# Performance work log

Hardware: AMD Instinct MI355X
Metric: run time of the kernel (lower is better)

## Reference

```python
import jax, jax.numpy as jnp
import numpy as np

B, S, D, H = 2, 2048, 1024, 16
DK = D // H


def setup_inputs() -> dict:
    key = jax.random.key(0)
    ks = jax.random.split(key, 7)
    return {
        "query": jax.random.normal(ks[0], (B, S, D), jnp.float32),
        "key": jax.random.normal(ks[1], (B, S, D), jnp.float32),
        "value": jax.random.normal(ks[2], (B, S, D), jnp.float32),
        "w_q": jax.random.normal(ks[3], (D, D), jnp.float32) * (1.0 / np.sqrt(D)),
        "w_k": jax.random.normal(ks[4], (D, D), jnp.float32) * (1.0 / np.sqrt(D)),
        "w_v": jax.random.normal(ks[5], (D, D), jnp.float32) * (1.0 / np.sqrt(D)),
        "w_o": jax.random.normal(ks[6], (D, D), jnp.float32) * (1.0 / np.sqrt(D)),
    }


def reference(query, key, value, w_q, w_k, w_v, w_o):
    # Linear(bias=False) in torch computes x @ W.T where W is [out, in].
    Q = jnp.einsum('bsd,ed->bse', query, w_q)
    K = jnp.einsum('bsd,ed->bse', key, w_k)
    V = jnp.einsum('bsd,ed->bse', value, w_v)
    # split heads: [B, H, S, DK]
    Q = Q.reshape(B, S, H, DK).transpose(0, 2, 1, 3)
    K = K.reshape(B, S, H, DK).transpose(0, 2, 1, 3)
    V = V.reshape(B, S, H, DK).transpose(0, 2, 1, 3)
    scale = 1.0 / np.sqrt(DK).astype(np.float32)
    scores = jnp.einsum('bhqd,bhkd->bhqk', Q, K) * scale  # [B,H,S,S]
    attn = jax.nn.softmax(scores, axis=-1)
    context = jnp.einsum('bhqk,bhkd->bhqd', attn, V)
    context = context.transpose(0, 2, 1, 3).reshape(B, S, D)
    return jnp.einsum('bsd,ed->bse', context, w_o)
```

## Files before the change

kernel.cpp:

```cpp
#include <hip/hip_runtime.h>

typedef unsigned short u16;
typedef unsigned int u32;
typedef __bf16 bf16x8 __attribute__((ext_vector_type(8)));
typedef float f32x4 __attribute__((ext_vector_type(4)));
typedef short s16x4 __attribute__((ext_vector_type(4)));

#define AS1 __attribute__((address_space(1)))
#define AS3 __attribute__((address_space(3)))

__device__ __forceinline__ f32x4 mfma16(bf16x8 a, bf16x8 b, f32x4 c) {
    return __builtin_amdgcn_mfma_f32_16x16x32_bf16(a, b, c, 0, 0, 0);
}
__device__ __forceinline__ f32x4 mfma16k16(s16x4 a, s16x4 b, f32x4 c) {
    return __builtin_amdgcn_mfma_f32_16x16x16bf16_1k(a, b, c, 0, 0, 0);
}

__device__ __forceinline__ u16 f2bf(float f) {
    return __builtin_bit_cast(u16, (__bf16)f);
}

__device__ __forceinline__ void gld16(const u16* g, u16* l) {
    __builtin_amdgcn_global_load_lds((AS1 void*)g, (AS3 void*)l, 16, 0, 0);
}

__global__ __launch_bounds__(256) void cvt_all(const float* __restrict__ q, const float* __restrict__ k,
                                               const float* __restrict__ v, const float* __restrict__ wq,
                                               const float* __restrict__ wk, const float* __restrict__ wv,
                                               const float* __restrict__ wo, u16* __restrict__ qo,
                                               u16* __restrict__ ko, u16* __restrict__ vo,
                                               u16* __restrict__ wqo, u16* __restrict__ wko,
                                               u16* __restrict__ wvo, u16* __restrict__ woo) {
    const int y = blockIdx.y;
    const float* x; u16* o; int n;
    switch (y) {
        case 0: x = q; o = qo; n = 4 << 20; break;
        case 1: x = k; o = ko; n = 4 << 20; break;
        case 2: x = v; o = vo; n = 4 << 20; break;
        case 3: x = wq; o = wqo; n = 1 << 20; break;
        case 4: x = wk; o = wko; n = 1 << 20; break;
        case 5: x = wv; o = wvo; n = 1 << 20; break;
        default: x = wo; o = woo; n = 1 << 20; break;
    }
    int i = (blockIdx.x * 256 + threadIdx.x) * 4;
    if (i >= n) return;
    float4 vv = *(const float4*)(x + i);
    u32 lo = (u32)f2bf(vv.x) | ((u32)f2bf(vv.y) << 16);
    u32 hi = (u32)f2bf(vv.z) | ((u32)f2bf(vv.w) << 16);
    *(uint2*)(o + i) = make_uint2(lo, hi);
}

template <int BM, int BN, bool BF16OUT>
__device__ __forceinline__ void gemm_core(const u16* __restrict__ A, const u16* __restrict__ Bt,
                                          void* __restrict__ Cp, int K, int N, int m0, int n0,
                                          float oscale) {
    constexpr int WROWS = BM / 64;
    constexpr int WCOLS = 4 / WROWS;
    constexpr int BFR = BN / WCOLS / 16;
    __shared__ __align__(16) u16 As[BM * 32];
    __shared__ __align__(16) u16 Bs[BN * 32];
    const int tid = threadIdx.x;
    const int lane = tid & 63, wave = tid >> 6;
    const int l16 = lane & 15, q4 = lane >> 4;
    const int wm = (wave / WCOLS) * 64, wn = (wave % WCOLS) * (BFR * 16);

    const f32x4 fz = {0.f, 0.f, 0.f, 0.f};
    f32x4 acc[4][BFR];
#pragma unroll
    for (int i = 0; i < 4; ++i)
#pragma unroll
        for (int j = 0; j < BFR; ++j) acc[i][j] = fz;

    const int rseg = lane >> 2;
    const int ck = ((lane & 3) ^ ((lane >> 3) & 3)) * 8;
    const u16* Ag = A + (size_t)(m0 + wave * 16 + rseg) * K + ck;
    const u16* Bg = Bt + (size_t)(n0 + wave * 16 + rseg) * K + ck;

    const int swz = (q4 ^ ((l16 & 7) >> 1)) * 8;

    for (int k0 = 0; k0 < K; k0 += 32) {
        __syncthreads();
#pragma unroll
        for (int p = 0; p < BM / 64; ++p)
            gld16(Ag + (size_t)p * 64 * K + k0, As + p * 2048 + wave * 512);
#pragma unroll
        for (int p = 0; p < BN / 64; ++p)
            gld16(Bg + (size_t)p * 64 * K + k0, Bs + p * 2048 + wave * 512);
        __syncthreads();
        bf16x8 af[4], bfr[BFR];
#pragma unroll
        for (int i = 0; i < 4; ++i)
            af[i] = *(const bf16x8*)&As[(wm + i * 16 + l16) * 32 + swz];
#pragma unroll
        for (int j = 0; j < BFR; ++j)
            bfr[j] = *(const bf16x8*)&Bs[(wn + j * 16 + l16) * 32 + swz];
#pragma unroll
        for (int i = 0; i < 4; ++i)
#pragma unroll
            for (int j = 0; j < BFR; ++j) acc[i][j] = mfma16(af[i], bfr[j], acc[i][j]);
    }

#pragma unroll
    for (int i = 0; i < 4; ++i) {
        const int row = m0 + wm + i * 16 + q4 * 4;
#pragma unroll
        for (int j = 0; j < BFR; ++j) {
            const int col = n0 + wn + j * 16 + l16;
#pragma unroll
            for (int r = 0; r < 4; ++r) {
                const float vr = acc[i][j][r] * oscale;
                if constexpr (BF16OUT)
                    ((u16*)Cp)[(size_t)(row + r) * N + col] = f2bf(vr);
                else
                    ((float*)Cp)[(size_t)(row + r) * N + col] = vr;
            }
        }
    }
}

__global__ __launch_bounds__(256) void gemm_qkv(const u16* __restrict__ qb, const u16* __restrict__ kb,
                                                const u16* __restrict__ vb, const u16* __restrict__ wqb,
                                                const u16* __restrict__ wkb, const u16* __restrict__ wvb,
                                                u16* __restrict__ Qp, u16* __restrict__ Kp,
                                                u16* __restrict__ VtAll) {
    const int z = blockIdx.y, x = blockIdx.x;
    const u16 *A, *Bt;
    u16* C;
    int N, m0, n0;
    float sc = 1.0f;
    if (z == 0) {
        A = qb; Bt = wqb; C = Qp; N = 1024; m0 = (x >> 3) * 128; n0 = (x & 7) * 128;
        sc = 0.18033688011112042f;
    } else if (z == 1) {
        A = kb; Bt = wkb; C = Kp; N = 1024; m0 = (x >> 3) * 128; n0 = (x & 7) * 128;
    } else {
        A = wvb; Bt = vb; C = VtAll; N = 4096; m0 = (x >> 5) * 128; n0 = (x & 31) * 128;
    }
    gemm_core<128, 128, true>(A, Bt, C, 1024, N, m0, n0, sc);
}

__global__ __launch_bounds__(256) void gemm_out(const u16* __restrict__ ctx,
                                                const u16* __restrict__ wob,
                                                float* __restrict__ out) {
    const int x = blockIdx.x;
    gemm_core<64, 128, false>(ctx, wob, out, 1024, 1024, (x >> 3) * 64, (x & 7) * 128, 1.0f);
}

__global__ __launch_bounds__(256) void flash_attn(const u16* __restrict__ Qp,
                                                  const u16* __restrict__ Kp,
                                                  const u16* __restrict__ VtAll,
                                                  float* __restrict__ Op0,
                                                  float* __restrict__ Op1,
                                                  float* __restrict__ Lp,
                                                  int NS, int ktLen) {
    constexpr int D = 1024, SS = 2048, LD = 72;
    __shared__ __align__(16) u16 Ks[64 * LD];
    __shared__ __align__(16) u16 Vts[64 * LD];

    const int tid = threadIdx.x;
    const int lane = tid & 63, wave = tid >> 6;
    const int l16 = lane & 15, q4 = lane >> 4;
    const int h = blockIdx.y;
    const int b = blockIdx.z / NS, half = blockIdx.z - b * NS;
    const int q0 = blockIdx.x * 128 + wave * 32;
    const int kt0 = half * ktLen, ktEnd = kt0 + ktLen;

    bf16x8 qf[2][2];
#pragma unroll
    for (int qs = 0; qs < 2; ++qs) {
        const u16* Qb = Qp + (size_t)(b * SS + q0 + qs * 16 + l16) * D + h * 64;
        qf[qs][0] = *(const bf16x8*)(Qb + q4 * 8);
        qf[qs][1] = *(const bf16x8*)(Qb + 32 + q4 * 8);
    }

    const f32x4 fz = {0.f, 0.f, 0.f, 0.f};
    f32x4 ot[2][4], lacc[2];
    lacc[0] = fz; lacc[1] = fz;
#pragma unroll
    for (int qs = 0; qs < 2; ++qs)
#pragma unroll
        for (int dt = 0; dt < 4; ++dt) ot[qs][dt] = fz;

    s16x4 onesA;
    onesA[0] = onesA[1] = onesA[2] = onesA[3] = (short)0x3F80;

    const int sr = tid >> 3, scol = (tid & 7) * 8;
    const int vswap = wave & 1;
    const int swV = (l16 >> 3) & 1;
    const u16* Kg = Kp + (size_t)(b * SS + sr) * D + h * 64 + scol;
    const u16* Vg = VtAll + (size_t)(h * 64 + sr) * 4096 + b * SS + scol;

    uint4 k0v = *(const uint4*)(Kg + (size_t)kt0 * D);
    uint4 k1v = *(const uint4*)(Kg + (size_t)(kt0 + 32) * D);
    uint4 v0v = *(const uint4*)(Vg + kt0);
    uint4 v1v = *(const uint4*)(Vg + (size_t)32 * 4096 + kt0);

    for (int kt = kt0; kt < ktEnd; kt += 64) {
        if (vswap) {
            v0v = make_uint4(v0v.z, v0v.w, v0v.x, v0v.y);
            v1v = make_uint4(v1v.z, v1v.w, v1v.x, v1v.y);
        }
        __syncthreads();
        *(uint4*)&Ks[sr * LD + scol] = k0v;
        *(uint4*)&Ks[(sr + 32) * LD + scol] = k1v;
        *(uint4*)&Vts[sr * LD + scol] = v0v;
        *(uint4*)&Vts[(sr + 32) * LD + scol] = v1v;
        __syncthreads();

        const int nk = (kt + 64 < ktEnd) ? kt + 64 : kt0;
        k0v = *(const uint4*)(Kg + (size_t)nk * D);
        k1v = *(const uint4*)(Kg + (size_t)(nk + 32) * D);
        v0v = *(const uint4*)(Vg + nk);
        v1v = *(const uint4*)(Vg + (size_t)32 * 4096 + nk);

        f32x4 st[2][4];
#pragma unroll
        for (int nt = 0; nt < 4; ++nt) {
            const bf16x8 ka = *(const bf16x8*)&Ks[(nt * 16 + l16) * LD + q4 * 8];
            const bf16x8 kbf = *(const bf16x8*)&Ks[(nt * 16 + l16) * LD + 32 + q4 * 8];
#pragma unroll
            for (int qs = 0; qs < 2; ++qs) {
                f32x4 s = mfma16(ka, qf[qs][0], fz);
                st[qs][nt] = mfma16(kbf, qf[qs][1], s);
            }
        }
        s16x4 p[2][4];
#pragma unroll
        for (int qs = 0; qs < 2; ++qs)
#pragma unroll
            for (int nt = 0; nt < 4; ++nt) {
                s16x4 pk;
#pragma unroll
                for (int r = 0; r < 4; ++r)
                    pk[r] = (short)f2bf(__builtin_amdgcn_exp2f(st[qs][nt][r]));
                p[qs][nt] = pk;
            }
#pragma unroll
        for (int nt = 0; nt < 4; ++nt) {
#pragma unroll
            for (int dt = 0; dt < 4; ++dt) {
                const s16x4 va = *(const s16x4*)&Vts[(dt * 16 + l16) * LD + ((nt * 4 + q4) ^ swV) * 4];
                ot[0][dt] = mfma16k16(va, p[0][nt], ot[0][dt]);
                ot[1][dt] = mfma16k16(va, p[1][nt], ot[1][dt]);
            }
            lacc[0] = mfma16k16(onesA, p[0][nt], lacc[0]);
            lacc[1] = mfma16k16(onesA, p[1][nt], lacc[1]);
        }
    }

    float* Op = half ? Op1 : Op0;
#pragma unroll
    for (int qs = 0; qs < 2; ++qs) {
        const int q = q0 + qs * 16 + l16;
        float* orow = Op + (size_t)(b * SS + q) * 1024 + h * 64;
#pragma unroll
        for (int dt = 0; dt < 4; ++dt)
            *(f32x4*)(orow + dt * 16 + q4 * 4) = ot[qs][dt];
        if (lane < 16)
            Lp[((half * 2 + b) * 16 + h) * 2048 + q] = lacc[qs][0];
    }
}

__global__ __launch_bounds__(256) void combine(const float* __restrict__ Op0,
                                               const float* __restrict__ Op1,
                                               const float* __restrict__ Lp,
                                               u16* __restrict__ ctx, int NS) {
    const int t = blockIdx.x * 256 + threadIdx.x;
    const int e = t * 4;
    const int d = e & 1023, bq = e >> 10;
    const int h = d >> 6, b = bq >> 11, q = bq & 2047;
    f32x4 o = *(const f32x4*)(Op0 + (size_t)bq * 1024 + d);
    float l = Lp[(b * 16 + h) * 2048 + q];
    if (NS == 2) {
        o += *(const f32x4*)(Op1 + (size_t)bq * 1024 + d);
        l += Lp[((2 + b) * 16 + h) * 2048 + q];
    }
    const float inv = 1.f / l;
    s16x4 w;
#pragma unroll
    for (int r = 0; r < 4; ++r) w[r] = (short)f2bf(o[r] * inv);
    *(s16x4*)(ctx + (size_t)bq * 1024 + d) = w;
}

extern "C" void kernel_launch(void* const* d_in, const int* in_sizes, int n_in,
                              void* d_out, int out_size, void* d_ws, size_t ws_size,
                              hipStream_t stream) {
    const float* query = (const float*)d_in[0];
    const float* key   = (const float*)d_in[1];
    const float* value = (const float*)d_in[2];
    const float* w_q   = (const float*)d_in[3];
    const float* w_k   = (const float*)d_in[4];
    const float* w_v   = (const float*)d_in[5];
    const float* w_o   = (const float*)d_in[6];
    float* out = (float*)d_out;

    const size_t MEG = 1024 * 1024;
    if (ws_size < 64 * MEG) return;
    u16* ws = (u16*)d_ws;
    u16* qb    = ws;
    u16* kb    = ws + 4 * MEG;
    u16* vb    = ws + 8 * MEG;
    u16* wqb   = ws + 12 * MEG;
    u16* wkb   = ws + 13 * MEG;
    u16* wvb   = ws + 14 * MEG;
    u16* wob   = ws + 15 * MEG;
    u16* Qp    = ws + 16 * MEG;
    u16* Kp    = ws + 20 * MEG;
    u16* VtAll = ws + 24 * MEG;
    u16* ctx   = ws + 28 * MEG;

    float* Op0 = (float*)ws;
    float* Lp  = (float*)(ws + 12 * MEG);
    float* Op1 = (float*)(ws + 32 * MEG);

    const int NS = (ws_size >= 80 * MEG) ? 2 : 1;
    const int ktLen = 2048 / NS;

    cvt_all<<<dim3(4096, 7), 256, 0, stream>>>(query, key, value, w_q, w_k, w_v, w_o,
                                               qb, kb, vb, wqb, wkb, wvb, wob);
    gemm_qkv<<<dim3(256, 3), 256, 0, stream>>>(qb, kb, vb, wqb, wkb, wvb, Qp, Kp, VtAll);
    flash_attn<<<dim3(16, 16, 2 * NS), 256, 0, stream>>>(Qp, Kp, VtAll, Op0, Op1, Lp, NS, ktLen);
    combine<<<dim3(4096), 256, 0, stream>>>(Op0, Op1, Lp, ctx, NS);
    gemm_out<<<dim3(512), 256, 0, stream>>>(ctx, wob, out);
}
```

Before: 229.3 us.

## Fuse softmax normalization into flash attention, drop KV split, double-buffer LDS

Removes the split-K attention mode and the separate combine kernel, so each block walks the full key range and writes the normalized bf16 context directly. The K/V shared tiles become double-buffered, which removes one barrier per iteration. This avoids writing and re-reading fp32 partial outputs and removes one kernel launch. The cost is half as many attention blocks (512 instead of 1024 when the workspace is large), which lowers parallelism on the GPU.

Result: faster. 217.3 us (-5.2%).

```diff
diff --git a/kernel.cpp b/kernel.cpp
--- a/kernel.cpp
+++ b/kernel.cpp
@@ -149,21 +149,16 @@
 __global__ __launch_bounds__(256) void flash_attn(const u16* __restrict__ Qp,
                                                   const u16* __restrict__ Kp,
                                                   const u16* __restrict__ VtAll,
-                                                  float* __restrict__ Op0,
-                                                  float* __restrict__ Op1,
-                                                  float* __restrict__ Lp,
-                                                  int NS, int ktLen) {
+                                                  u16* __restrict__ Ctx) {
     constexpr int D = 1024, SS = 2048, LD = 72;
-    __shared__ __align__(16) u16 Ks[64 * LD];
-    __shared__ __align__(16) u16 Vts[64 * LD];
+    __shared__ __align__(16) u16 Ks[2][64 * LD];
+    __shared__ __align__(16) u16 Vts[2][64 * LD];
 
     const int tid = threadIdx.x;
     const int lane = tid & 63, wave = tid >> 6;
     const int l16 = lane & 15, q4 = lane >> 4;
-    const int h = blockIdx.y;
-    const int b = blockIdx.z / NS, half = blockIdx.z - b * NS;
+    const int h = blockIdx.y, b = blockIdx.z;
     const int q0 = blockIdx.x * 128 + wave * 32;
-    const int kt0 = half * ktLen, ktEnd = kt0 + ktLen;
 
     bf16x8 qf[2][2];
 #pragma unroll
@@ -190,34 +185,36 @@
     const u16* Kg = Kp + (size_t)(b * SS + sr) * D + h * 64 + scol;
     const u16* Vg = VtAll + (size_t)(h * 64 + sr) * 4096 + b * SS + scol;
 
-    uint4 k0v = *(const uint4*)(Kg + (size_t)kt0 * D);
-    uint4 k1v = *(const uint4*)(Kg + (size_t)(kt0 + 32) * D);
-    uint4 v0v = *(const uint4*)(Vg + kt0);
-    uint4 v1v = *(const uint4*)(Vg + (size_t)32 * 4096 + kt0);
-
-    for (int kt = kt0; kt < ktEnd; kt += 64) {
+    uint4 k0v = *(const uint4*)(Kg);
+    uint4 k1v = *(const uint4*)(Kg + (size_t)32 * D);
+    uint4 v0v = *(const uint4*)(Vg);
+    uint4 v1v = *(const uint4*)(Vg + (size_t)32 * 4096);
+
+    for (int kt = 0; kt < SS; kt += 64) {
+        const int buf = (kt >> 6) & 1;
+        uint4 w0 = v0v, w1 = v1v;
         if (vswap) {
-            v0v = make_uint4(v0v.z, v0v.w, v0v.x, v0v.y);
-            v1v = make_uint4(v1v.z, v1v.w, v1v.x, v1v.y);
-        }
-        __syncthreads();
-        *(uint4*)&Ks[sr * LD + scol] = k0v;
-        *(uint4*)&Ks[(sr + 32) * LD + scol] = k1v;
-        *(uint4*)&Vts[sr * LD + scol] = v0v;
-        *(uint4*)&Vts[(sr + 32) * LD + scol] = v1v;
-        __syncthreads();
-
-        const int nk = (kt + 64 < ktEnd) ? kt + 64 : kt0;
+            w0 = make_uint4(v0v.z, v0v.w, v0v.x, v0v.y);
+            w1 = make_uint4(v1v.z, v1v.w, v1v.x, v1v.y);
+        }
+        *(uint4*)&Ks[buf][sr * LD + scol] = k0v;
+        *(uint4*)&Ks[buf][(sr + 32) * LD + scol] = k1v;
+        *(uint4*)&Vts[buf][sr * LD + scol] = w0;
+        *(uint4*)&Vts[buf][(sr + 32) * LD + scol] = w1;
+
+        const int nk = (kt + 64 < SS) ? kt + 64 : 0;
         k0v = *(const uint4*)(Kg + (size_t)nk * D);
         k1v = *(const uint4*)(Kg + (size_t)(nk + 32) * D);
         v0v = *(const uint4*)(Vg + nk);
         v1v = *(const uint4*)(Vg + (size_t)32 * 4096 + nk);
 
+        __syncthreads();
+
         f32x4 st[2][4];
 #pragma unroll
         for (int nt = 0; nt < 4; ++nt) {
-            const bf16x8 ka = *(const bf16x8*)&Ks[(nt * 16 + l16) * LD + q4 * 8];
-            const bf16x8 kbf = *(const bf16x8*)&Ks[(nt * 16 + l16) * LD + 32 + q4 * 8];
+            const bf16x8 ka = *(const bf16x8*)&Ks[buf][(nt * 16 + l16) * LD + q4 * 8];
+            const bf16x8 kbf = *(const bf16x8*)&Ks[buf][(nt * 16 + l16) * LD + 32 + q4 * 8];
 #pragma unroll
             for (int qs = 0; qs < 2; ++qs) {
                 f32x4 s = mfma16(ka, qf[qs][0], fz);
@@ -239,7 +236,8 @@
         for (int nt = 0; nt < 4; ++nt) {
 #pragma unroll
             for (int dt = 0; dt < 4; ++dt) {
-                const s16x4 va = *(const s16x4*)&Vts[(dt * 16 + l16) * LD + ((nt * 4 + q4) ^ swV) * 4];
+                const s16x4 va =
+                    *(const s16x4*)&Vts[buf][(dt * 16 + l16) * LD + ((nt * 4 + q4) ^ swV) * 4];
                 ot[0][dt] = mfma16k16(va, p[0][nt], ot[0][dt]);
                 ot[1][dt] = mfma16k16(va, p[1][nt], ot[1][dt]);
             }
@@ -248,38 +246,18 @@
         }
     }
 
-    float* Op = half ? Op1 : Op0;
 #pragma unroll
     for (int qs = 0; qs < 2; ++qs) {
-        const int q = q0 + qs * 16 + l16;
-        float* orow = Op + (size_t)(b * SS + q) * 1024 + h * 64;
-#pragma unroll
-        for (int dt = 0; dt < 4; ++dt)
-            *(f32x4*)(orow + dt * 16 + q4 * 4) = ot[qs][dt];
-        if (lane < 16)
-            Lp[((half * 2 + b) * 16 + h) * 2048 + q] = lacc[qs][0];
-    }
-}
-
-__global__ __launch_bounds__(256) void combine(const float* __restrict__ Op0,
-                                               const float* __restrict__ Op1,
-                                               const float* __restrict__ Lp,
-                                               u16* __restrict__ ctx, int NS) {
-    const int t = blockIdx.x * 256 + threadIdx.x;
-    const int e = t * 4;
-    const int d = e & 1023, bq = e >> 10;
-    const int h = d >> 6, b = bq >> 11, q = bq & 2047;
-    f32x4 o = *(const f32x4*)(Op0 + (size_t)bq * 1024 + d);
-    float l = Lp[(b * 16 + h) * 2048 + q];
-    if (NS == 2) {
-        o += *(const f32x4*)(Op1 + (size_t)bq * 1024 + d);
-        l += Lp[((2 + b) * 16 + h) * 2048 + q];
-    }
-    const float inv = 1.f / l;
-    s16x4 w;
-#pragma unroll
-    for (int r = 0; r < 4; ++r) w[r] = (short)f2bf(o[r] * inv);
-    *(s16x4*)(ctx + (size_t)bq * 1024 + d) = w;
+        const float inv = 1.f / lacc[qs][0];
+        u16* Cb = Ctx + (size_t)(b * SS + q0 + qs * 16 + l16) * D + h * 64 + q4 * 4;
+#pragma unroll
+        for (int dt = 0; dt < 4; ++dt) {
+            s16x4 w;
+#pragma unroll
+            for (int r = 0; r < 4; ++r) w[r] = (short)f2bf(ot[qs][dt][r] * inv);
+            *(s16x4*)(Cb + dt * 16) = w;
+        }
+    }
 }
 
 extern "C" void kernel_launch(void* const* d_in, const int* in_sizes, int n_in,
@@ -309,17 +287,9 @@
     u16* VtAll = ws + 24 * MEG;
     u16* ctx   = ws + 28 * MEG;
 
-    float* Op0 = (float*)ws;
-    float* Lp  = (float*)(ws + 12 * MEG);
-    float* Op1 = (float*)(ws + 32 * MEG);
-
-    const int NS = (ws_size >= 80 * MEG) ? 2 : 1;
-    const int ktLen = 2048 / NS;
-
     cvt_all<<<dim3(4096, 7), 256, 0, stream>>>(query, key, value, w_q, w_k, w_v, w_o,
                                                qb, kb, vb, wqb, wkb, wvb, wob);
     gemm_qkv<<<dim3(256, 3), 256, 0, stream>>>(qb, kb, vb, wqb, wkb, wvb, Qp, Kp, VtAll);
-    flash_attn<<<dim3(16, 16, 2 * NS), 256, 0, stream>>>(Qp, Kp, VtAll, Op0, Op1, Lp, NS, ktLen);
-    combine<<<dim3(4096), 256, 0, stream>>>(Op0, Op1, Lp, ctx, NS);
+    flash_attn<<<dim3(16, 16, 2), 256, 0, stream>>>(Qp, Kp, VtAll, ctx);
     gemm_out<<<dim3(512), 256, 0, stream>>>(ctx, wob, out);
 }
```
